# Kernel tuning notes

Hardware: AMD Instinct MI355X
Metric: run time of the kernel (lower is better)

## Reference

```python
import jax, jax.numpy as jnp
import numpy as np

O_FEATURES = 4096
I_FEATURES = 4096
N_TOKENS = 8192


def _unpack_int4(packed, out_shape):
    # packed: int32 holding uint8 byte values; two signed int4 per byte (offset-8)
    p = packed.astype(jnp.int32)
    even = (p & 15) - 8          # low nibble
    odd = ((p >> 4) & 15) - 8    # high nibble
    # interleave: stacked[0::2] = even, stacked[1::2] = odd
    stacked = jnp.stack([even, odd], axis=-1).reshape(-1)
    return stacked.reshape(out_shape)


def setup_inputs() -> dict:
    key = jax.random.key(0)
    k1, k2, k3 = jax.random.split(key, 3)
    x = jax.random.normal(k1, (N_TOKENS, I_FEATURES), dtype=jnp.float32)
    packed_w = jax.random.randint(k2, (O_FEATURES * I_FEATURES // 2,), 0, 256, dtype=jnp.int32)
    # per-output-channel scale (positive, as produced by abs-max / qmax)
    scale = jax.random.uniform(k3, (O_FEATURES, 1), dtype=jnp.float32) * 0.01 + 1e-4
    return {"x": x, "packed_w": packed_w, "scale": scale}


def reference(x, packed_w, scale):
    # dequantize: unpack int4 -> target dtype, multiply per-row scale
    int_w = _unpack_int4(packed_w, (O_FEATURES, I_FEATURES)).astype(x.dtype)  # [O, I]
    w = int_w * scale.astype(x.dtype)  # scale broadcasts [O,1] over [O,I]
    # downstream quantized linear: y = x @ W^T
    return jnp.einsum('ni,oi->no', x, w)
```

## Files before the change

kernel.cpp:

```cpp
#include <hip/hip_runtime.h>

typedef unsigned char u8;
typedef signed char s8;
typedef unsigned int u32;
typedef __attribute__((ext_vector_type(4))) int i32x4;

#define M_TOK 8192
#define N_OUT 4096
#define K_IN  4096
#define NT    32

static __device__ __forceinline__ u32 pack4(float4 v, float inv) {
    int q0 = __float2int_rn(v.x * inv) & 255;
    int q1 = __float2int_rn(v.y * inv) & 255;
    int q2 = __float2int_rn(v.z * inv) & 255;
    int q3 = __float2int_rn(v.w * inv) & 255;
    return (u32)q0 | ((u32)q1 << 8) | ((u32)q2 << 16) | ((u32)q3 << 24);
}

__global__ __launch_bounds__(256) void prep_kernel(const float* __restrict__ x,
                                                   const int* __restrict__ pw,
                                                   s8* __restrict__ xq,
                                                   float* __restrict__ sx,
                                                   s8* __restrict__ wq) {
    int bid = blockIdx.x;
    int t = threadIdx.x;
    if (bid < 2048) {
        int row = bid * 4 + (t >> 6);
        int ln = t & 63;
        const float4* xr = (const float4*)(x + (size_t)row * K_IN);
        float4 v[16];
        float am = 0.f;
#pragma unroll
        for (int j = 0; j < 16; ++j) {
            v[j] = xr[ln + j * 64];
            am = fmaxf(am, fmaxf(fmaxf(fabsf(v[j].x), fabsf(v[j].y)),
                                 fmaxf(fabsf(v[j].z), fabsf(v[j].w))));
        }
#pragma unroll
        for (int o = 32; o > 0; o >>= 1) am = fmaxf(am, __shfl_xor(am, o));
        float inv = (am > 0.f) ? 127.f / am : 0.f;
        if (ln == 0) sx[row] = (am > 0.f) ? am / 127.f : 0.f;
        u32* out = (u32*)(xq + (size_t)row * K_IN);
#pragma unroll
        for (int j = 0; j < 16; ++j) out[ln + j * 64] = pack4(v[j], inv);
    } else {
        const int n4 = (N_OUT * K_IN / 2) / 4;
        int idx = (bid - 2048) * 256 + t;
        const int stride = 512 * 256;
        for (int i = idx; i < n4; i += stride) {
            int4 p = *(const int4*)(pw + (size_t)i * 4);
            u32 lo = (u32)(((p.x & 15) - 8) & 255)
                   | ((u32)((((p.x >> 4) & 15) - 8) & 255) << 8)
                   | ((u32)((((p.y) & 15) - 8) & 255) << 16)
                   | ((u32)((((p.y >> 4) & 15) - 8) & 255) << 24);
            u32 hi = (u32)(((p.z & 15) - 8) & 255)
                   | ((u32)((((p.z >> 4) & 15) - 8) & 255) << 8)
                   | ((u32)((((p.w) & 15) - 8) & 255) << 16)
                   | ((u32)((((p.w >> 4) & 15) - 8) & 255) << 24);
            uint2 o; o.x = lo; o.y = hi;
            *(uint2*)(wq + (size_t)i * 8) = o;
        }
    }
}

#define MFMA(a, b, c) __builtin_amdgcn_mfma_i32_16x16x64_i8(a, b, c, 0, 0, 0)

static __device__ __forceinline__ i32x4 ldsv(const u8* p, int idx) {
    return *(const i32x4*)(p + idx);
}

#define MFMA16(A00, A01, A10, A11, M0, M1)                \
    acc[M0][0] = MFMA(A00, b00, acc[M0][0]);              \
    acc[M0][1] = MFMA(A00, b10, acc[M0][1]);              \
    acc[M0][2] = MFMA(A00, b20, acc[M0][2]);              \
    acc[M0][3] = MFMA(A00, b30, acc[M0][3]);              \
    acc[M1][0] = MFMA(A10, b00, acc[M1][0]);              \
    acc[M1][1] = MFMA(A10, b10, acc[M1][1]);              \
    acc[M1][2] = MFMA(A10, b20, acc[M1][2]);              \
    acc[M1][3] = MFMA(A10, b30, acc[M1][3]);              \
    acc[M0][0] = MFMA(A01, b01, acc[M0][0]);              \
    acc[M0][1] = MFMA(A01, b11, acc[M0][1]);              \
    acc[M0][2] = MFMA(A01, b21, acc[M0][2]);              \
    acc[M0][3] = MFMA(A01, b31, acc[M0][3]);              \
    acc[M1][0] = MFMA(A11, b01, acc[M1][0]);              \
    acc[M1][1] = MFMA(A11, b11, acc[M1][1]);              \
    acc[M1][2] = MFMA(A11, b21, acc[M1][2]);              \
    acc[M1][3] = MFMA(A11, b31, acc[M1][3]);

__global__ __launch_bounds__(512, 2) void gemmra_i8_kernel(const s8* __restrict__ A,
                                                           const s8* __restrict__ B,
                                                           const float* __restrict__ sx,
                                                           const float* __restrict__ scale,
                                                           float* __restrict__ C) {
    __shared__ __align__(16) u8 lds[131072];

#define GLo(src, dstIdx)                                                        \
    __builtin_amdgcn_global_load_lds(                                           \
        (const __attribute__((address_space(1))) void*)(src),                   \
        (__attribute__((address_space(3))) void*)&lds[dstIdx], 16, 0, 0)

    int wg = blockIdx.x;
    int swz = (wg & 7) * 64 + (wg >> 3);
    int bm = swz >> 4;
    int bn = swz & 15;

    int t = threadIdx.x;
    int l = t & 63;
    int wid = t >> 6;
    int wr = wid >> 2;
    int wc = wid & 3;

    const size_t soff = (size_t)(t >> 3) * K_IN + (size_t)((((t & 7) ^ ((t >> 3) & 7)) << 4));
    const size_t S64 = (size_t)64 * K_IN;
    const int t16 = t * 16;

    const s8* Alo = A + (size_t)(bm * 256) * K_IN;
    const s8* Ahi = Alo + (size_t)128 * K_IN;
    const s8* Blo = B + (size_t)(bn * 256) * K_IN;
    const s8* Bhi = Blo + (size_t)128 * K_IN;

    const int kx = (l & 7) << 4;
    const int koff0 = (((l >> 4) << 4)) ^ kx;
    const int koff1 = koff0 ^ 64;
    const int aB = wr * 16384 + (l & 15) * 128;
    const int bB = 32768 + wc * 8192 + (l & 15) * 128;

    i32x4 acc[8][4] = {};

    GLo(Blo + soff, 32768 + t16);         GLo(Blo + soff + S64, 32768 + t16 + 8192);
    GLo(Bhi + soff, 49152 + t16);         GLo(Bhi + soff + S64, 49152 + t16 + 8192);
    GLo(Alo + soff, t16);                 GLo(Alo + soff + S64, t16 + 8192);
    GLo(Ahi + soff, 16384 + t16);         GLo(Ahi + soff + S64, 16384 + t16 + 8192);
    GLo(Blo + soff + 128, 98304 + t16);   GLo(Blo + soff + S64 + 128, 98304 + t16 + 8192);
    GLo(Bhi + soff + 128, 114688 + t16);  GLo(Bhi + soff + S64 + 128, 114688 + t16 + 8192);
    asm volatile("s_waitcnt vmcnt(4)" ::: "memory");
    __builtin_amdgcn_s_barrier();

    for (int T = 0; T < NT; ++T) {
        const int buf = T & 1;
        const u8* L = lds + buf * 65536;

        i32x4 b00 = ldsv(L, bB + koff0),        b01 = ldsv(L, bB + koff1);
        i32x4 b10 = ldsv(L, bB + 2048 + koff0), b11 = ldsv(L, bB + 2048 + koff1);
        i32x4 b20 = ldsv(L, bB + 4096 + koff0), b21 = ldsv(L, bB + 4096 + koff1);
        i32x4 b30 = ldsv(L, bB + 6144 + koff0), b31 = ldsv(L, bB + 6144 + koff1);
        i32x4 p00 = ldsv(L, aB + koff0),        p01 = ldsv(L, aB + koff1);
        i32x4 p10 = ldsv(L, aB + 2048 + koff0), p11 = ldsv(L, aB + 2048 + koff1);

        if (T + 1 < NT) {
            size_t ko = (size_t)(T + 1) * 128;
            int d = (buf ^ 1) * 65536 + t16;
            GLo(Alo + soff + ko, d);                 GLo(Alo + soff + S64 + ko, d + 8192);
            GLo(Ahi + soff + ko, d + 16384);         GLo(Ahi + soff + S64 + ko, d + 24576);
        }

        i32x4 q00 = ldsv(L, aB + 4096 + koff0), q01 = ldsv(L, aB + 4096 + koff1);
        i32x4 q10 = ldsv(L, aB + 6144 + koff0), q11 = ldsv(L, aB + 6144 + koff1);

        __builtin_amdgcn_s_setprio(1);
        MFMA16(p00, p01, p10, p11, 0, 1);
        __builtin_amdgcn_s_setprio(0);

        p00 = ldsv(L, aB + 8192 + koff0);  p01 = ldsv(L, aB + 8192 + koff1);
        p10 = ldsv(L, aB + 10240 + koff0); p11 = ldsv(L, aB + 10240 + koff1);

        __builtin_amdgcn_s_setprio(1);
        MFMA16(q00, q01, q10, q11, 2, 3);
        __builtin_amdgcn_s_setprio(0);

        __builtin_amdgcn_s_barrier();
        asm volatile("" ::: "memory");

        if (T + 2 < NT) {
            size_t ko = (size_t)(T + 2) * 128;
            int d = buf * 65536 + 32768 + t16;
            GLo(Blo + soff + ko, d);          GLo(Blo + soff + S64 + ko, d + 8192);
            GLo(Bhi + soff + ko, d + 16384);  GLo(Bhi + soff + S64 + ko, d + 24576);
        }

        q00 = ldsv(L, aB + 12288 + koff0); q01 = ldsv(L, aB + 12288 + koff1);
        q10 = ldsv(L, aB + 14336 + koff0); q11 = ldsv(L, aB + 14336 + koff1);

        __builtin_amdgcn_s_setprio(1);
        MFMA16(p00, p01, p10, p11, 4, 5);
        MFMA16(q00, q01, q10, q11, 6, 7);
        __builtin_amdgcn_s_setprio(0);

        if (T < NT - 2) asm volatile("s_waitcnt vmcnt(4)" ::: "memory");
        else            asm volatile("s_waitcnt vmcnt(0)" ::: "memory");
        __builtin_amdgcn_s_barrier();
    }

    int col0 = bn * 256 + wc * 64 + (l & 15);
    float sc_[4];
#pragma unroll
    for (int n = 0; n < 4; ++n) sc_[n] = scale[col0 + n * 16];

#pragma unroll
    for (int m = 0; m < 8; ++m) {
        int row0 = bm * 256 + wr * 128 + m * 16 + (l >> 4) * 4;
        float4 sxr = *(const float4*)(sx + row0);
        float sxa[4] = {sxr.x, sxr.y, sxr.z, sxr.w};
#pragma unroll
        for (int n = 0; n < 4; ++n) {
            int gcol = col0 + n * 16;
#pragma unroll
            for (int j = 0; j < 4; ++j)
                C[(size_t)(row0 + j) * N_OUT + gcol] = (float)acc[m][n][j] * sxa[j] * sc_[n];
        }
    }
#undef GLo
}

__global__ __launch_bounds__(256) void gemm_fb_kernel(const float* __restrict__ X,
                                                      const int* __restrict__ PW,
                                                      const float* __restrict__ S,
                                                      float* __restrict__ C) {
    __shared__ float sxm[64][33];
    __shared__ float swm[64][33];
    int bm = blockIdx.x / (N_OUT / 64);
    int bn = blockIdx.x % (N_OUT / 64);
    int t = threadIdx.x;
    int r = t >> 2, c8 = (t & 3) * 8;
    int tx = t & 15, ty = t >> 4;
    float acc[4][4] = {};
    for (int k0 = 0; k0 < K_IN; k0 += 32) {
        const float* xs = X + (size_t)(bm * 64 + r) * K_IN + k0 + c8;
#pragma unroll
        for (int j = 0; j < 8; ++j) sxm[r][c8 + j] = xs[j];
        const int* ps = PW + ((size_t)(bn * 64 + r) * K_IN + k0 + c8) / 2;
#pragma unroll
        for (int j = 0; j < 4; ++j) {
            int b = ps[j];
            swm[r][c8 + 2 * j]     = (float)((b & 15) - 8);
            swm[r][c8 + 2 * j + 1] = (float)(((b >> 4) & 15) - 8);
        }
        __syncthreads();
#pragma unroll
        for (int kk = 0; kk < 32; ++kk) {
            float a[4], w[4];
#pragma unroll
            for (int i = 0; i < 4; ++i) a[i] = sxm[ty * 4 + i][kk];
#pragma unroll
            for (int j = 0; j < 4; ++j) w[j] = swm[tx * 4 + j][kk];
#pragma unroll
            for (int i = 0; i < 4; ++i)
#pragma unroll
                for (int j = 0; j < 4; ++j) acc[i][j] += a[i] * w[j];
        }
        __syncthreads();
    }
#pragma unroll
    for (int i = 0; i < 4; ++i) {
        int gr = bm * 64 + ty * 4 + i;
#pragma unroll
        for (int j = 0; j < 4; ++j) {
            int gc = bn * 64 + tx * 4 + j;
            C[(size_t)gr * N_OUT + gc] = acc[i][j] * S[gc];
        }
    }
}

extern "C" void kernel_launch(void* const* d_in, const int* in_sizes, int n_in,
                              void* d_out, int out_size, void* d_ws, size_t ws_size,
                              hipStream_t stream) {
    const float* x  = (const float*)d_in[0];
    const int*   pw = (const int*)d_in[1];
    const float* sc = (const float*)d_in[2];
    float* out = (float*)d_out;

    const size_t xq_bytes = (size_t)M_TOK * K_IN;
    const size_t wq_bytes = (size_t)N_OUT * K_IN;
    const size_t sx_bytes = (size_t)M_TOK * sizeof(float);
    const size_t need = xq_bytes + wq_bytes + sx_bytes;

    if (ws_size >= need) {
        s8* xq = (s8*)d_ws;
        s8* wq = xq + xq_bytes;
        float* sx = (float*)(wq + wq_bytes);
        prep_kernel<<<dim3(2560), dim3(256), 0, stream>>>(x, pw, xq, sx, wq);
        gemmra_i8_kernel<<<dim3((M_TOK / 256) * (N_OUT / 256)), dim3(512), 0, stream>>>(
            xq, wq, sx, sc, out);
    } else {
        gemm_fb_kernel<<<dim3((M_TOK / 64) * (N_OUT / 64)), dim3(256), 0, stream>>>(x, pw, sc, out);
    }
}
```

Baseline: 169.3 us.

## Make GEMM blocks persistent over two M tiles, overlapping next prologue with epilogue

The int8 GEMM now launches 256 workgroups instead of 512, and each one processes two consecutive 256-row M tiles against the same N tile. The global-to-LDS prologue loads for the second tile are issued before the first tile's epilogue stores, so the stores overlap the prefetch and a second wave of workgroup launches is avoided. In exchange the grid is halved, which means 256 blocks at two per CU on a 256-CU part. Any load imbalance or tail stalls now cover twice the work per block.

```diff
diff --git a/kernel.cpp b/kernel.cpp
--- a/kernel.cpp
+++ b/kernel.cpp
@@ -88,7 +88,7 @@
     acc[M1][2] = MFMA(A11, b21, acc[M1][2]);              \
     acc[M1][3] = MFMA(A11, b31, acc[M1][3]);
 
-__global__ __launch_bounds__(512, 2) void gemmra_i8_kernel(const s8* __restrict__ A,
+__global__ __launch_bounds__(512, 2) void gemmx2_i8_kernel(const s8* __restrict__ A,
                                                            const s8* __restrict__ B,
                                                            const float* __restrict__ sx,
                                                            const float* __restrict__ scale,
@@ -101,9 +101,9 @@
         (__attribute__((address_space(3))) void*)&lds[dstIdx], 16, 0, 0)
 
     int wg = blockIdx.x;
-    int swz = (wg & 7) * 64 + (wg >> 3);
-    int bm = swz >> 4;
-    int bn = swz & 15;
+    int swz = (wg & 7) * 32 + (wg >> 3);
+    int bn  = swz & 15;
+    int bm0 = (swz >> 4) * 2;
 
     int t = threadIdx.x;
     int l = t & 63;
@@ -115,8 +115,6 @@
     const size_t S64 = (size_t)64 * K_IN;
     const int t16 = t * 16;
 
-    const s8* Alo = A + (size_t)(bm * 256) * K_IN;
-    const s8* Ahi = Alo + (size_t)128 * K_IN;
     const s8* Blo = B + (size_t)(bn * 256) * K_IN;
     const s8* Bhi = Blo + (size_t)128 * K_IN;
 
@@ -126,90 +124,117 @@
     const int aB = wr * 16384 + (l & 15) * 128;
     const int bB = 32768 + wc * 8192 + (l & 15) * 128;
 
-    i32x4 acc[8][4] = {};
-
-    GLo(Blo + soff, 32768 + t16);         GLo(Blo + soff + S64, 32768 + t16 + 8192);
-    GLo(Bhi + soff, 49152 + t16);         GLo(Bhi + soff + S64, 49152 + t16 + 8192);
-    GLo(Alo + soff, t16);                 GLo(Alo + soff + S64, t16 + 8192);
-    GLo(Ahi + soff, 16384 + t16);         GLo(Ahi + soff + S64, 16384 + t16 + 8192);
-    GLo(Blo + soff + 128, 98304 + t16);   GLo(Blo + soff + S64 + 128, 98304 + t16 + 8192);
-    GLo(Bhi + soff + 128, 114688 + t16);  GLo(Bhi + soff + S64 + 128, 114688 + t16 + 8192);
+#define PROSTAGE(APlo, APhi)                                                      \
+    do {                                                                          \
+        GLo(Blo + soff, 32768 + t16);         GLo(Blo + soff + S64, 32768 + t16 + 8192); \
+        GLo(Bhi + soff, 49152 + t16);         GLo(Bhi + soff + S64, 49152 + t16 + 8192); \
+        GLo((APlo) + soff, t16);              GLo((APlo) + soff + S64, t16 + 8192);      \
+        GLo((APhi) + soff, 16384 + t16);      GLo((APhi) + soff + S64, 16384 + t16 + 8192); \
+        GLo(Blo + soff + 128, 98304 + t16);   GLo(Blo + soff + S64 + 128, 98304 + t16 + 8192); \
+        GLo(Bhi + soff + 128, 114688 + t16);  GLo(Bhi + soff + S64 + 128, 114688 + t16 + 8192); \
+    } while (0)
+
+    {
+        const s8* A0lo = A + (size_t)(bm0 * 256) * K_IN;
+        const s8* A0hi = A0lo + (size_t)128 * K_IN;
+        PROSTAGE(A0lo, A0hi);
+    }
     asm volatile("s_waitcnt vmcnt(4)" ::: "memory");
     __builtin_amdgcn_s_barrier();
 
-    for (int T = 0; T < NT; ++T) {
-        const int buf = T & 1;
-        const u8* L = lds + buf * 65536;
-
-        i32x4 b00 = ldsv(L, bB + koff0),        b01 = ldsv(L, bB + koff1);
-        i32x4 b10 = ldsv(L, bB + 2048 + koff0), b11 = ldsv(L, bB + 2048 + koff1);
-        i32x4 b20 = ldsv(L, bB + 4096 + koff0), b21 = ldsv(L, bB + 4096 + koff1);
-        i32x4 b30 = ldsv(L, bB + 6144 + koff0), b31 = ldsv(L, bB + 6144 + koff1);
-        i32x4 p00 = ldsv(L, aB + koff0),        p01 = ldsv(L, aB + koff1);
-        i32x4 p10 = ldsv(L, aB + 2048 + koff0), p11 = ldsv(L, aB + 2048 + koff1);
-
-        if (T + 1 < NT) {
-            size_t ko = (size_t)(T + 1) * 128;
-            int d = (buf ^ 1) * 65536 + t16;
-            GLo(Alo + soff + ko, d);                 GLo(Alo + soff + S64 + ko, d + 8192);
-            GLo(Ahi + soff + ko, d + 16384);         GLo(Ahi + soff + S64 + ko, d + 24576);
-        }
-
-        i32x4 q00 = ldsv(L, aB + 4096 + koff0), q01 = ldsv(L, aB + 4096 + koff1);
-        i32x4 q10 = ldsv(L, aB + 6144 + koff0), q11 = ldsv(L, aB + 6144 + koff1);
-
-        __builtin_amdgcn_s_setprio(1);
-        MFMA16(p00, p01, p10, p11, 0, 1);
-        __builtin_amdgcn_s_setprio(0);
-
-        p00 = ldsv(L, aB + 8192 + koff0);  p01 = ldsv(L, aB + 8192 + koff1);
-        p10 = ldsv(L, aB + 10240 + koff0); p11 = ldsv(L, aB + 10240 + koff1);
-
-        __builtin_amdgcn_s_setprio(1);
-        MFMA16(q00, q01, q10, q11, 2, 3);
-        __builtin_amdgcn_s_setprio(0);
-
-        __builtin_amdgcn_s_barrier();
-        asm volatile("" ::: "memory");
-
-        if (T + 2 < NT) {
-            size_t ko = (size_t)(T + 2) * 128;
-            int d = buf * 65536 + 32768 + t16;
-            GLo(Blo + soff + ko, d);          GLo(Blo + soff + S64 + ko, d + 8192);
-            GLo(Bhi + soff + ko, d + 16384);  GLo(Bhi + soff + S64 + ko, d + 24576);
-        }
-
-        q00 = ldsv(L, aB + 12288 + koff0); q01 = ldsv(L, aB + 12288 + koff1);
-        q10 = ldsv(L, aB + 14336 + koff0); q11 = ldsv(L, aB + 14336 + koff1);
-
-        __builtin_amdgcn_s_setprio(1);
-        MFMA16(p00, p01, p10, p11, 4, 5);
-        MFMA16(q00, q01, q10, q11, 6, 7);
-        __builtin_amdgcn_s_setprio(0);
-
-        if (T < NT - 2) asm volatile("s_waitcnt vmcnt(4)" ::: "memory");
-        else            asm volatile("s_waitcnt vmcnt(0)" ::: "memory");
-        __builtin_amdgcn_s_barrier();
-    }
-
-    int col0 = bn * 256 + wc * 64 + (l & 15);
-    float sc_[4];
-#pragma unroll
-    for (int n = 0; n < 4; ++n) sc_[n] = scale[col0 + n * 16];
-
-#pragma unroll
-    for (int m = 0; m < 8; ++m) {
-        int row0 = bm * 256 + wr * 128 + m * 16 + (l >> 4) * 4;
-        float4 sxr = *(const float4*)(sx + row0);
-        float sxa[4] = {sxr.x, sxr.y, sxr.z, sxr.w};
-#pragma unroll
-        for (int n = 0; n < 4; ++n) {
-            int gcol = col0 + n * 16;
-#pragma unroll
-            for (int j = 0; j < 4; ++j)
-                C[(size_t)(row0 + j) * N_OUT + gcol] = (float)acc[m][n][j] * sxa[j] * sc_[n];
-        }
-    }
+    for (int p = 0; p < 2; ++p) {
+        const int bm = bm0 + p;
+        const s8* Alo = A + (size_t)(bm * 256) * K_IN;
+        const s8* Ahi = Alo + (size_t)128 * K_IN;
+
+        i32x4 acc[8][4] = {};
+
+        for (int T = 0; T < NT; ++T) {
+            const int buf = T & 1;
+            const u8* L = lds + buf * 65536;
+
+            i32x4 b00 = ldsv(L, bB + koff0),        b01 = ldsv(L, bB + koff1);
+            i32x4 b10 = ldsv(L, bB + 2048 + koff0), b11 = ldsv(L, bB + 2048 + koff1);
+            i32x4 b20 = ldsv(L, bB + 4096 + koff0), b21 = ldsv(L, bB + 4096 + koff1);
+            i32x4 b30 = ldsv(L, bB + 6144 + koff0), b31 = ldsv(L, bB + 6144 + koff1);
+            i32x4 p00 = ldsv(L, aB + koff0),        p01 = ldsv(L, aB + koff1);
+            i32x4 p10 = ldsv(L, aB + 2048 + koff0), p11 = ldsv(L, aB + 2048 + koff1);
+
+            if (T + 1 < NT) {
+                size_t ko = (size_t)(T + 1) * 128;
+                int d = (buf ^ 1) * 65536 + t16;
+                GLo(Alo + soff + ko, d);                 GLo(Alo + soff + S64 + ko, d + 8192);
+                GLo(Ahi + soff + ko, d + 16384);         GLo(Ahi + soff + S64 + ko, d + 24576);
+            }
+
+            i32x4 q00 = ldsv(L, aB + 4096 + koff0), q01 = ldsv(L, aB + 4096 + koff1);
+            i32x4 q10 = ldsv(L, aB + 6144 + koff0), q11 = ldsv(L, aB + 6144 + koff1);
+
+            __builtin_amdgcn_s_setprio(1);
+            MFMA16(p00, p01, p10, p11, 0, 1);
+            __builtin_amdgcn_s_setprio(0);
+
+            p00 = ldsv(L, aB + 8192 + koff0);  p01 = ldsv(L, aB + 8192 + koff1);
+            p10 = ldsv(L, aB + 10240 + koff0); p11 = ldsv(L, aB + 10240 + koff1);
+
+            __builtin_amdgcn_s_setprio(1);
+            MFMA16(q00, q01, q10, q11, 2, 3);
+            __builtin_amdgcn_s_setprio(0);
+
+            __builtin_amdgcn_s_barrier();
+            asm volatile("" ::: "memory");
+
+            if (T + 2 < NT) {
+                size_t ko = (size_t)(T + 2) * 128;
+                int d = buf * 65536 + 32768 + t16;
+                GLo(Blo + soff + ko, d);          GLo(Blo + soff + S64 + ko, d + 8192);
+                GLo(Bhi + soff + ko, d + 16384);  GLo(Bhi + soff + S64 + ko, d + 24576);
+            }
+
+            q00 = ldsv(L, aB + 12288 + koff0); q01 = ldsv(L, aB + 12288 + koff1);
+            q10 = ldsv(L, aB + 14336 + koff0); q11 = ldsv(L, aB + 14336 + koff1);
+
+            __builtin_amdgcn_s_setprio(1);
+            MFMA16(p00, p01, p10, p11, 4, 5);
+            MFMA16(q00, q01, q10, q11, 6, 7);
+            __builtin_amdgcn_s_setprio(0);
+
+            if (T < NT - 2) asm volatile("s_waitcnt vmcnt(4)" ::: "memory");
+            else            asm volatile("s_waitcnt vmcnt(0)" ::: "memory");
+            __builtin_amdgcn_s_barrier();
+        }
+
+        if (p == 0) {
+            const s8* A1lo = A + (size_t)((bm0 + 1) * 256) * K_IN;
+            const s8* A1hi = A1lo + (size_t)128 * K_IN;
+            PROSTAGE(A1lo, A1hi);
+        }
+
+        int col0 = bn * 256 + wc * 64 + (l & 15);
+        float sc_[4];
+#pragma unroll
+        for (int n = 0; n < 4; ++n) sc_[n] = scale[col0 + n * 16];
+
+#pragma unroll
+        for (int m = 0; m < 8; ++m) {
+            int row0 = bm * 256 + wr * 128 + m * 16 + (l >> 4) * 4;
+            float4 sxr = *(const float4*)(sx + row0);
+            float sxa[4] = {sxr.x, sxr.y, sxr.z, sxr.w};
+#pragma unroll
+            for (int n = 0; n < 4; ++n) {
+                int gcol = col0 + n * 16;
+#pragma unroll
+                for (int j = 0; j < 4; ++j)
+                    C[(size_t)(row0 + j) * N_OUT + gcol] = (float)acc[m][n][j] * sxa[j] * sc_[n];
+            }
+        }
+
+        if (p == 0) {
+            asm volatile("s_waitcnt vmcnt(0)" ::: "memory");
+            __builtin_amdgcn_s_barrier();
+        }
+    }
+#undef PROSTAGE
 #undef GLo
 }
 
@@ -280,8 +305,7 @@
         s8* wq = xq + xq_bytes;
         float* sx = (float*)(wq + wq_bytes);
         prep_kernel<<<dim3(2560), dim3(256), 0, stream>>>(x, pw, xq, sx, wq);
-        gemmra_i8_kernel<<<dim3((M_TOK / 256) * (N_OUT / 256)), dim3(512), 0, stream>>>(
-            xq, wq, sx, sc, out);
+        gemmx2_i8_kernel<<<dim3(256), dim3(512), 0, stream>>>(xq, wq, sx, sc, out);
     } else {
         gemm_fb_kernel<<<dim3((M_TOK / 64) * (N_OUT / 64)), dim3(256), 0, stream>>>(x, pw, sc, out);
     }
```

Result: no change. 171.1 us (+1.1%).
